# Performance work log

Measured on AMD Instinct MI355X. Metric: run time of the kernel, lower is better.

## Reference

```python
import jax, jax.numpy as jnp
import numpy as np

D_MODEL = 1024
PATCH = 16
HID = 256
VOCAB = 256

def setup_inputs() -> dict:
    key = jax.random.key(0)
    ks = jax.random.split(key, 12)
    B, N = 16, 512
    s = lambda *sh: 1.0 / np.sqrt(sh[-1])
    inp = {
        'latents': jax.random.normal(ks[0], (B, N, D_MODEL), dtype=jnp.float32),
        'target_bytes': jax.random.randint(ks[1], (B, N * PATCH), 0, VOCAB, dtype=jnp.int64),
        'W_proj': jax.random.normal(ks[2], (HID, D_MODEL), dtype=jnp.float32) * s(HID, D_MODEL),
        'b_proj': jnp.zeros((HID,), dtype=jnp.float32),
        'emb_table': jax.random.normal(ks[3], (VOCAB, HID), dtype=jnp.float32),
        'W_ih': jax.random.normal(ks[4], (3 * HID, 2 * HID), dtype=jnp.float32) * s(1, 2 * HID),
        'W_hh': jax.random.normal(ks[5], (3 * HID, HID), dtype=jnp.float32) * s(1, HID),
        'b_ih': jnp.zeros((3 * HID,), dtype=jnp.float32),
        'b_hh': jnp.zeros((3 * HID,), dtype=jnp.float32),
        'W_head': jax.random.normal(ks[6], (VOCAB, HID), dtype=jnp.float32) * s(VOCAB, HID),
        'b_head': jnp.zeros((VOCAB,), dtype=jnp.float32),
    }
    return inp

def _gru_scan(x_proj, W_hh, b_hh, h0):
    # x_proj: [T, BN, 3H] precomputed input projections (incl. b_ih)
    def step(h, xg):
        hg = h @ W_hh.T + b_hh                      # [BN, 3H]
        xr, xz, xn = jnp.split(xg, 3, axis=-1)
        hr, hz, hn = jnp.split(hg, 3, axis=-1)
        r = jax.nn.sigmoid(xr + hr)
        z = jax.nn.sigmoid(xz + hz)
        n = jnp.tanh(xn + r * hn)
        h_new = (1.0 - z) * n + z * h
        return h_new, h_new
    _, outs = jax.lax.scan(step, h0, x_proj)
    return outs                                      # [T, BN, H]

def reference(latents, target_bytes, W_proj, b_proj, emb_table, W_ih, W_hh, b_ih, b_hh, W_head, b_head):
    B, N, D = latents.shape
    BN = B * N
    latent_ctx = (latents.reshape(BN, D) @ W_proj.T + b_proj)        # [BN, H]
    targets = target_bytes.reshape(BN, PATCH)
    sos = jnp.zeros((BN, 1), dtype=targets.dtype)
    rnn_in_bytes = jnp.concatenate([sos, targets[:, :-1]], axis=1)   # [BN, P]
    emb = emb_table[rnn_in_bytes]                                    # [BN, P, H]
    lat_exp = jnp.broadcast_to(latent_ctx[:, None, :], (BN, PATCH, HID))
    rnn_input = jnp.concatenate([emb, lat_exp], axis=-1)             # [BN, P, 2H]
    x_proj = jnp.einsum('bpi,gi->bpg', rnn_input, W_ih) + b_ih       # [BN, P, 3H]
    h0 = jnp.zeros((BN, HID), dtype=latents.dtype)
    outs = _gru_scan(jnp.swapaxes(x_proj, 0, 1), W_hh, b_hh, h0)     # [P, BN, H]
    outs = jnp.swapaxes(outs, 0, 1)                                  # [BN, P, H]
    logits = jnp.einsum('bph,vh->bpv', outs, W_head) + b_head        # [BN, P, 256]
    return logits.reshape(B, N, PATCH, VOCAB)
```

## Files before the change

### kernel.cpp

```cpp
#include <hip/hip_runtime.h>
#include <math.h>

#define NSEQ 8192
#define PATCHL 16
#define HIDN 256
#define VOCABN 256

typedef __attribute__((ext_vector_type(4))) float f32x4;
typedef __attribute__((ext_vector_type(8))) short bf16x8;

__device__ __forceinline__ unsigned short f2bf(float f) {
    unsigned int x = __float_as_uint(f);
    unsigned int r = (x + 0x7fffu + ((x >> 16) & 1u)) >> 16;
    return (unsigned short)r;
}
__device__ __forceinline__ float bf2f(unsigned short b) {
    return __uint_as_float(((unsigned int)b) << 16);
}
__device__ __forceinline__ float sigf(float x)   { return 1.f / (1.f + __expf(-x)); }
__device__ __forceinline__ float tanhf_(float x) { return 2.f / (1.f + __expf(-2.f * x)) - 1.f; }

__global__ __launch_bounds__(256)
void pack_frag(const float* __restrict__ src, int ld, int col0, int nks,
               unsigned short* __restrict__ dst)
{
    const int g = blockIdx.x * 256 + threadIdx.x;
    const int lane = g & 63;
    const int ks = (g / 64) % nks;
    const int T  = g / (64 * nks);
    const float* s = src + (size_t)(T * 16 + (lane & 15)) * ld + col0 + ks * 32 + ((lane >> 4) & 3) * 8;
    unsigned int q[4];
#pragma unroll
    for (int j = 0; j < 4; j++) {
        unsigned int lo = f2bf(s[2 * j]);
        unsigned int hi = f2bf(s[2 * j + 1]);
        q[j] = lo | (hi << 16);
    }
    uint4 v; v.x = q[0]; v.y = q[1]; v.z = q[2]; v.w = q[3];
    *(uint4*)(dst + (size_t)g * 8) = v;
}

template<bool ASRC_BF16, int OUT_MODE>
__global__ __launch_bounds__(512)
void gemm_mfma(const void* __restrict__ Asrc, int lda,
               const unsigned short* __restrict__ bpack, int nks_total,
               const float* __restrict__ bias, void* __restrict__ Cdst, int ldc,
               int K)
{
    const int tid = threadIdx.x;
    const int w = tid >> 6, lane = tid & 63;
    const int l15 = lane & 15, kg = (lane >> 4) & 3;
    const int bm = blockIdx.x * 128, bn = blockIdx.y * 64;

    __shared__ unsigned short As[2][128 * 64];

    const int srow = tid >> 2;
    const int scol = (tid & 3) * 16;
    const int nkt = K / 64;

    f32x4 acc[4];
#pragma unroll
    for (int nt = 0; nt < 4; nt++) acc[nt] = 0.f;

    const int wb0 = srow * 128 + ((scol * 2) ^ ((srow & 7) << 4));
    const int wb1 = srow * 128 + ((scol * 2 + 16) ^ ((srow & 7) << 4));

#define STAGE(kt, buf) do {                                                         \
        const int gk = (kt) * 64 + scol;                                            \
        unsigned short tmp[16];                                                     \
        if (ASRC_BF16) {                                                            \
            const unsigned short* A = (const unsigned short*)Asrc;                  \
            *(uint4*)(tmp)     = *(const uint4*)(A + (size_t)(bm + srow) * lda + gk);      \
            *(uint4*)(tmp + 8) = *(const uint4*)(A + (size_t)(bm + srow) * lda + gk + 8);  \
        } else {                                                                    \
            const float* A = (const float*)Asrc;                                    \
            const float4 a0 = *(const float4*)(A + (size_t)(bm + srow) * lda + gk);       \
            const float4 a1 = *(const float4*)(A + (size_t)(bm + srow) * lda + gk + 4);   \
            const float4 a2 = *(const float4*)(A + (size_t)(bm + srow) * lda + gk + 8);   \
            const float4 a3 = *(const float4*)(A + (size_t)(bm + srow) * lda + gk + 12);  \
            tmp[0] = f2bf(a0.x);  tmp[1] = f2bf(a0.y);  tmp[2] = f2bf(a0.z);  tmp[3] = f2bf(a0.w);   \
            tmp[4] = f2bf(a1.x);  tmp[5] = f2bf(a1.y);  tmp[6] = f2bf(a1.z);  tmp[7] = f2bf(a1.w);   \
            tmp[8] = f2bf(a2.x);  tmp[9] = f2bf(a2.y);  tmp[10] = f2bf(a2.z); tmp[11] = f2bf(a2.w);  \
            tmp[12] = f2bf(a3.x); tmp[13] = f2bf(a3.y); tmp[14] = f2bf(a3.z); tmp[15] = f2bf(a3.w);  \
        }                                                                           \
        *(uint4*)((char*)As[buf] + wb0) = *(uint4*)tmp;                             \
        *(uint4*)((char*)As[buf] + wb1) = *(uint4*)(tmp + 8);                       \
    } while (0)

    STAGE(0, 0);
    __syncthreads();

    for (int kt = 0; kt < nkt; ++kt) {
        if (kt + 1 < nkt) STAGE(kt + 1, (kt + 1) & 1);
        const unsigned short* buf = As[kt & 1];
        const int row = w * 16 + l15;
#pragma unroll
        for (int ks = 0; ks < 2; ++ks) {
            const int bo = row * 128 + (((ks * 64) + kg * 16) ^ ((row & 7) << 4));
            const bf16x8 a = *(const bf16x8*)((const char*)buf + bo);
#pragma unroll
            for (int nt = 0; nt < 4; ++nt) {
                const int T = blockIdx.y * 4 + nt;
                const bf16x8 b = *(const bf16x8*)(bpack + (((size_t)T * nks_total + (kt * 2 + ks)) * 64 + lane) * 8);
                acc[nt] = __builtin_amdgcn_mfma_f32_16x16x32_bf16(a, b, acc[nt], 0, 0, 0);
            }
        }
        __syncthreads();
    }
#undef STAGE

#pragma unroll
    for (int nt = 0; nt < 4; ++nt) {
        const int n = bn + nt * 16 + l15;
        const float bv = bias ? bias[n] : 0.f;
#pragma unroll
        for (int rr = 0; rr < 4; ++rr) {
            const int m = bm + w * 16 + kg * 4 + rr;
            const float v = acc[nt][rr] + bv;
            if (OUT_MODE == 0)      ((float*)Cdst)[(size_t)m * ldc + n] = v;
            else if (OUT_MODE == 1) ((unsigned short*)Cdst)[(size_t)m * ldc + n] = f2bf(v);
            else                    ((unsigned short*)Cdst)[(size_t)m * 1024 + (n & 255) * 4 + (n >> 8)] = f2bf(v);
        }
    }
}

#define G4S 1032
__global__ __launch_bounds__(512)
void gru_scan_fused(const int* __restrict__ bytes,
                    const unsigned short* __restrict__ latg4,
                    const unsigned short* __restrict__ pmx4,
                    const unsigned short* __restrict__ wpack,
                    const unsigned short* __restrict__ hpack,
                    const float* __restrict__ b_hh,
                    const float* __restrict__ b_head,
                    float* __restrict__ out)
{
    const int tid  = threadIdx.x;
    const int w    = tid >> 6;
    const int lane = tid & 63;
    const int l15  = lane & 15;
    const int kg   = (lane >> 4) & 3;
    const int s0   = blockIdx.x * 32;

    __shared__ unsigned short H0[32 * 256];
    __shared__ unsigned short H1[32 * 256];
    __shared__ unsigned short LG[32 * G4S];
    __shared__ int BYs[512];

    BYs[tid] = bytes[(size_t)s0 * PATCHL + tid];

#pragma unroll
    for (int j = 0; j < 8; ++j) {
        const int idx = j * 512 + tid;
        const int row = idx >> 7, col = idx & 127;
        *(uint4*)(LG + row * G4S + col * 8) =
            *(const uint4*)(latg4 + (size_t)(s0 + row) * 1024 + col * 8);
    }

    float bhr[2], bhz[2], bhn[2], bhd[2];
#pragma unroll
    for (int nt = 0; nt < 2; nt++) {
        const int u = w * 32 + nt * 16 + l15;
        bhr[nt] = b_hh[u]; bhz[nt] = b_hh[256 + u]; bhn[nt] = b_hh[512 + u];
        bhd[nt] = b_head[u];
    }

    float hreg[2][2][4];
#pragma unroll
    for (int mt = 0; mt < 2; mt++)
#pragma unroll
        for (int nt = 0; nt < 2; nt++)
#pragma unroll
            for (int rr = 0; rr < 4; rr++) hreg[mt][nt][rr] = 0.f;

    unsigned short* Hcur = H0;
    unsigned short* Hnxt = H1;

    __syncthreads();

#define MFMA_TILES(pk, tbase, Hb, acc) do {                                         \
        _Pragma("unroll")                                                           \
        for (int ks = 0; ks < 8; ks += 2) {                                         \
            bf16x8 B[2][2];                                                         \
            _Pragma("unroll")                                                       \
            for (int dk = 0; dk < 2; ++dk)                                          \
                _Pragma("unroll")                                                   \
                for (int nt = 0; nt < 2; ++nt) {                                    \
                    const int T = (tbase) + w * 2 + nt;                             \
                    B[dk][nt] = *(const bf16x8*)((pk) + (((size_t)T * 8 + ks + dk) * 64 + lane) * 8); \
                }                                                                   \
            _Pragma("unroll")                                                       \
            for (int dk = 0; dk < 2; ++dk)                                          \
                _Pragma("unroll")                                                   \
                for (int mt = 0; mt < 2; ++mt) {                                    \
                    const int s = mt * 16 + l15;                                    \
                    const int off = ((ks + dk) * 64 + kg * 16) ^ ((l15 & 7) << 4);  \
                    const bf16x8 a = *(const bf16x8*)((Hb) + s * 256 + (off >> 1)); \
                    _Pragma("unroll")                                               \
                    for (int nt = 0; nt < 2; ++nt)                                  \
                        acc[mt][nt] = __builtin_amdgcn_mfma_f32_16x16x32_bf16(a, B[dk][nt], acc[mt][nt], 0, 0, 0); \
                }                                                                   \
        }                                                                           \
    } while (0)

#define HEAD_STORE(pp, Hb) do {                                                     \
        f32x4 acch[2][2];                                                           \
        _Pragma("unroll")                                                           \
        for (int mt = 0; mt < 2; mt++)                                              \
            _Pragma("unroll")                                                       \
            for (int nt = 0; nt < 2; nt++) acch[mt][nt] = 0.f;                      \
        MFMA_TILES(hpack, 0, Hb, acch);                                             \
        _Pragma("unroll")                                                           \
        for (int mt = 0; mt < 2; mt++)                                              \
            _Pragma("unroll")                                                       \
            for (int nt = 0; nt < 2; nt++) {                                        \
                const int u = w * 32 + nt * 16 + l15;                               \
                _Pragma("unroll")                                                   \
                for (int rr = 0; rr < 4; rr++) {                                    \
                    const int sl = mt * 16 + kg * 4 + rr;                           \
                    out[((size_t)(s0 + sl) * PATCHL + (pp)) * VOCABN + u] =         \
                        acch[mt][nt][rr] + bhd[nt];                                 \
                }                                                                   \
            }                                                                       \
    } while (0)

    for (int p = 0; p < PATCHL; ++p) {
        ushort4 pmreg[2][2][4];
#pragma unroll
        for (int mt = 0; mt < 2; mt++)
#pragma unroll
            for (int nt = 0; nt < 2; nt++) {
                const int u = w * 32 + nt * 16 + l15;
#pragma unroll
                for (int rr = 0; rr < 4; rr++) {
                    const int sl = mt * 16 + kg * 4 + rr;
                    const int bv = p ? BYs[sl * PATCHL + p - 1] : 0;
                    pmreg[mt][nt][rr] = *(const ushort4*)(pmx4 + (size_t)bv * 1024 + u * 4);
                }
            }

        if (p) HEAD_STORE(p - 1, Hcur);

        f32x4 acc[2][2];
#pragma unroll
        for (int mt = 0; mt < 2; mt++)
#pragma unroll
            for (int nt = 0; nt < 2; nt++) acc[mt][nt] = 0.f;
        if (p) MFMA_TILES(wpack, 0, Hcur, acc);

        float rv[2][2][4], xz[2][2][4], xn[2][2][4];
#pragma unroll
        for (int mt = 0; mt < 2; mt++)
#pragma unroll
            for (int nt = 0; nt < 2; nt++) {
                const int u = w * 32 + nt * 16 + l15;
#pragma unroll
                for (int rr = 0; rr < 4; rr++) {
                    const int sl = mt * 16 + kg * 4 + rr;
                    const ushort4 lg4 = *(const ushort4*)(LG + sl * G4S + u * 4);
                    const ushort4 pm4 = pmreg[mt][nt][rr];
                    const float xr = bf2f(lg4.x) + bf2f(pm4.x) + bhr[nt];
                    rv[mt][nt][rr] = sigf(xr + acc[mt][nt][rr]);
                    xz[mt][nt][rr] = bf2f(lg4.y) + bf2f(pm4.y) + bhz[nt];
                    xn[mt][nt][rr] = bf2f(lg4.z) + bf2f(pm4.z);
                }
            }

#pragma unroll
        for (int mt = 0; mt < 2; mt++)
#pragma unroll
            for (int nt = 0; nt < 2; nt++) acc[mt][nt] = 0.f;
        if (p) MFMA_TILES(wpack, 16, Hcur, acc);

        float zv[2][2][4];
#pragma unroll
        for (int mt = 0; mt < 2; mt++)
#pragma unroll
            for (int nt = 0; nt < 2; nt++)
#pragma unroll
                for (int rr = 0; rr < 4; rr++)
                    zv[mt][nt][rr] = sigf(xz[mt][nt][rr] + acc[mt][nt][rr]);

#pragma unroll
        for (int mt = 0; mt < 2; mt++)
#pragma unroll
            for (int nt = 0; nt < 2; nt++) acc[mt][nt] = 0.f;
        if (p) MFMA_TILES(wpack, 32, Hcur, acc);

#pragma unroll
        for (int mt = 0; mt < 2; mt++)
#pragma unroll
            for (int nt = 0; nt < 2; nt++) {
                const int u = w * 32 + nt * 16 + l15;
#pragma unroll
                for (int rr = 0; rr < 4; rr++) {
                    const int sl = mt * 16 + kg * 4 + rr;
                    const float n = tanhf_(xn[mt][nt][rr] + rv[mt][nt][rr] * (acc[mt][nt][rr] + bhn[nt]));
                    const float hn_ = (1.f - zv[mt][nt][rr]) * n + zv[mt][nt][rr] * hreg[mt][nt][rr];
                    hreg[mt][nt][rr] = hn_;
                    const int bo = (2 * u) ^ ((sl & 7) << 4);
                    Hnxt[sl * 256 + (bo >> 1)] = f2bf(hn_);
                }
            }
        __syncthreads();
        unsigned short* t_ = Hcur; Hcur = Hnxt; Hnxt = t_;
    }

    HEAD_STORE(PATCHL - 1, Hcur);
#undef HEAD_STORE
#undef MFMA_TILES
}

extern "C" void kernel_launch(void* const* d_in, const int* in_sizes, int n_in,
                              void* d_out, int out_size, void* d_ws, size_t ws_size,
                              hipStream_t stream)
{
    const float* latents = (const float*)d_in[0];
    const int*   tb      = (const int*)d_in[1];
    const float* W_proj  = (const float*)d_in[2];
    const float* b_proj  = (const float*)d_in[3];
    const float* emb     = (const float*)d_in[4];
    const float* W_ih    = (const float*)d_in[5];
    const float* W_hh    = (const float*)d_in[6];
    const float* b_ih    = (const float*)d_in[7];
    const float* b_hh    = (const float*)d_in[8];
    const float* W_head  = (const float*)d_in[9];
    const float* b_head  = (const float*)d_in[10];
    float* out = (float*)d_out;

    char* w = (char*)d_ws;
    unsigned short* latg4   = (unsigned short*)w;          w += (size_t)NSEQ * 1024 * 2;
    unsigned short* ctxb    = (unsigned short*)w;          w += (size_t)NSEQ * HIDN * 2;
    unsigned short* pmx4    = (unsigned short*)w;          w += 256 * 1024 * 2;
    unsigned short* bpack1  = (unsigned short*)w;          w += 16 * 32 * 64 * 8 * 2;
    unsigned short* bpack2  = (unsigned short*)w;          w += 48 * 8 * 64 * 8 * 2;
    unsigned short* bpack3  = (unsigned short*)w;          w += 48 * 8 * 64 * 8 * 2;
    unsigned short* wpackG  = (unsigned short*)w;          w += 48 * 8 * 64 * 8 * 2;
    unsigned short* bpackH  = (unsigned short*)w;          w += 16 * 8 * 64 * 8 * 2;

    hipLaunchKernelGGL(pack_frag, dim3(128), dim3(256), 0, stream, W_proj, 1024, 0, 32, bpack1);
    hipLaunchKernelGGL(pack_frag, dim3(96),  dim3(256), 0, stream, W_ih,   512, 256, 8, bpack2);
    hipLaunchKernelGGL(pack_frag, dim3(96),  dim3(256), 0, stream, W_ih,   512, 0,   8, bpack3);
    hipLaunchKernelGGL(pack_frag, dim3(96),  dim3(256), 0, stream, W_hh,   256, 0,   8, wpackG);
    hipLaunchKernelGGL(pack_frag, dim3(32),  dim3(256), 0, stream, W_head, 256, 0,   8, bpackH);

    hipLaunchKernelGGL((gemm_mfma<false, 2>), dim3(2, 12), dim3(512), 0, stream,
                       emb, 256, bpack3, 8, nullptr, pmx4, 1024, 256);
    hipLaunchKernelGGL((gemm_mfma<false, 1>), dim3(NSEQ / 128, 4), dim3(512), 0, stream,
                       latents, 1024, bpack1, 32, b_proj, ctxb, 256, 1024);
    hipLaunchKernelGGL((gemm_mfma<true, 2>), dim3(NSEQ / 128, 12), dim3(512), 0, stream,
                       ctxb, 256, bpack2, 8, b_ih, latg4, 1024, 256);

    hipLaunchKernelGGL(gru_scan_fused, dim3(NSEQ / 32), dim3(512), 0, stream,
                       tb, latg4, pmx4, wpackG, bpackH, b_hh, b_head, out);
}
```

Before: 375.3 us.

## Shrink GRU scan blocks to 16 sequences with 4 waves per block

The fused GRU scan kernel now processes 16 sequences per block with 256 threads instead of 32 sequences with 512 threads. Each wave covers 64 hidden units (4 N-tiles) and a single 16-row M-tile, so each loaded weight fragment now feeds one A row-tile instead of two. The aim is to double the grid (512 blocks), cut LDS per block so more blocks fit per CU, and shorten the per-step barrier. The cost is that weight fragments are re-read from memory by twice as many blocks per step, with less reuse per load.

```diff
diff --git a/kernel.cpp b/kernel.cpp
--- a/kernel.cpp
+++ b/kernel.cpp
@@ -125,7 +125,7 @@
 }
 
 #define G4S 1032
-__global__ __launch_bounds__(512)
+__global__ __launch_bounds__(256)
 void gru_scan_fused(const int* __restrict__ bytes,
                     const unsigned short* __restrict__ latg4,
                     const unsigned short* __restrict__ pmx4,
@@ -140,38 +140,36 @@
     const int lane = tid & 63;
     const int l15  = lane & 15;
     const int kg   = (lane >> 4) & 3;
-    const int s0   = blockIdx.x * 32;
-
-    __shared__ unsigned short H0[32 * 256];
-    __shared__ unsigned short H1[32 * 256];
-    __shared__ unsigned short LG[32 * G4S];
-    __shared__ int BYs[512];
+    const int s0   = blockIdx.x * 16;
+
+    __shared__ unsigned short H0[16 * 256];
+    __shared__ unsigned short H1[16 * 256];
+    __shared__ unsigned short LG[16 * G4S];
+    __shared__ int BYs[256];
 
     BYs[tid] = bytes[(size_t)s0 * PATCHL + tid];
 
 #pragma unroll
     for (int j = 0; j < 8; ++j) {
-        const int idx = j * 512 + tid;
+        const int idx = j * 256 + tid;
         const int row = idx >> 7, col = idx & 127;
         *(uint4*)(LG + row * G4S + col * 8) =
             *(const uint4*)(latg4 + (size_t)(s0 + row) * 1024 + col * 8);
     }
 
-    float bhr[2], bhz[2], bhn[2], bhd[2];
-#pragma unroll
-    for (int nt = 0; nt < 2; nt++) {
-        const int u = w * 32 + nt * 16 + l15;
+    float bhr[4], bhz[4], bhn[4], bhd[4];
+#pragma unroll
+    for (int nt = 0; nt < 4; nt++) {
+        const int u = w * 64 + nt * 16 + l15;
         bhr[nt] = b_hh[u]; bhz[nt] = b_hh[256 + u]; bhn[nt] = b_hh[512 + u];
         bhd[nt] = b_head[u];
     }
 
-    float hreg[2][2][4];
-#pragma unroll
-    for (int mt = 0; mt < 2; mt++)
-#pragma unroll
-        for (int nt = 0; nt < 2; nt++)
-#pragma unroll
-            for (int rr = 0; rr < 4; rr++) hreg[mt][nt][rr] = 0.f;
+    float hreg[4][4];
+#pragma unroll
+    for (int nt = 0; nt < 4; nt++)
+#pragma unroll
+        for (int rr = 0; rr < 4; rr++) hreg[nt][rr] = 0.f;
 
     unsigned short* Hcur = H0;
     unsigned short* Hnxt = H1;
@@ -181,127 +179,106 @@
 #define MFMA_TILES(pk, tbase, Hb, acc) do {                                         \
         _Pragma("unroll")                                                           \
         for (int ks = 0; ks < 8; ks += 2) {                                         \
-            bf16x8 B[2][2];                                                         \
+            bf16x8 B[2][4];                                                         \
             _Pragma("unroll")                                                       \
             for (int dk = 0; dk < 2; ++dk)                                          \
                 _Pragma("unroll")                                                   \
-                for (int nt = 0; nt < 2; ++nt) {                                    \
-                    const int T = (tbase) + w * 2 + nt;                             \
+                for (int nt = 0; nt < 4; ++nt) {                                    \
+                    const int T = (tbase) + w * 4 + nt;                             \
                     B[dk][nt] = *(const bf16x8*)((pk) + (((size_t)T * 8 + ks + dk) * 64 + lane) * 8); \
                 }                                                                   \
             _Pragma("unroll")                                                       \
-            for (int dk = 0; dk < 2; ++dk)                                          \
+            for (int dk = 0; dk < 2; ++dk) {                                        \
+                const int off = ((ks + dk) * 64 + kg * 16) ^ ((l15 & 7) << 4);      \
+                const bf16x8 a = *(const bf16x8*)((Hb) + l15 * 256 + (off >> 1));   \
                 _Pragma("unroll")                                                   \
-                for (int mt = 0; mt < 2; ++mt) {                                    \
-                    const int s = mt * 16 + l15;                                    \
-                    const int off = ((ks + dk) * 64 + kg * 16) ^ ((l15 & 7) << 4);  \
-                    const bf16x8 a = *(const bf16x8*)((Hb) + s * 256 + (off >> 1)); \
-                    _Pragma("unroll")                                               \
-                    for (int nt = 0; nt < 2; ++nt)                                  \
-                        acc[mt][nt] = __builtin_amdgcn_mfma_f32_16x16x32_bf16(a, B[dk][nt], acc[mt][nt], 0, 0, 0); \
-                }                                                                   \
+                for (int nt = 0; nt < 4; ++nt)                                      \
+                    acc[nt] = __builtin_amdgcn_mfma_f32_16x16x32_bf16(a, B[dk][nt], acc[nt], 0, 0, 0); \
+            }                                                                       \
         }                                                                           \
     } while (0)
 
 #define HEAD_STORE(pp, Hb) do {                                                     \
-        f32x4 acch[2][2];                                                           \
+        f32x4 acch[4];                                                              \
         _Pragma("unroll")                                                           \
-        for (int mt = 0; mt < 2; mt++)                                              \
-            _Pragma("unroll")                                                       \
-            for (int nt = 0; nt < 2; nt++) acch[mt][nt] = 0.f;                      \
+        for (int nt = 0; nt < 4; nt++) acch[nt] = 0.f;                              \
         MFMA_TILES(hpack, 0, Hb, acch);                                             \
         _Pragma("unroll")                                                           \
-        for (int mt = 0; mt < 2; mt++)                                              \
+        for (int nt = 0; nt < 4; nt++) {                                            \
+            const int u = w * 64 + nt * 16 + l15;                                   \
             _Pragma("unroll")                                                       \
-            for (int nt = 0; nt < 2; nt++) {                                        \
-                const int u = w * 32 + nt * 16 + l15;                               \
-                _Pragma("unroll")                                                   \
-                for (int rr = 0; rr < 4; rr++) {                                    \
-                    const int sl = mt * 16 + kg * 4 + rr;                           \
-                    out[((size_t)(s0 + sl) * PATCHL + (pp)) * VOCABN + u] =         \
-                        acch[mt][nt][rr] + bhd[nt];                                 \
-                }                                                                   \
+            for (int rr = 0; rr < 4; rr++) {                                        \
+                const int sl = kg * 4 + rr;                                         \
+                out[((size_t)(s0 + sl) * PATCHL + (pp)) * VOCABN + u] =             \
+                    acch[nt][rr] + bhd[nt];                                         \
             }                                                                       \
+        }                                                                           \
     } while (0)
 
     for (int p = 0; p < PATCHL; ++p) {
-        ushort4 pmreg[2][2][4];
-#pragma unroll
-        for (int mt = 0; mt < 2; mt++)
-#pragma unroll
-            for (int nt = 0; nt < 2; nt++) {
-                const int u = w * 32 + nt * 16 + l15;
-#pragma unroll
-                for (int rr = 0; rr < 4; rr++) {
-                    const int sl = mt * 16 + kg * 4 + rr;
-                    const int bv = p ? BYs[sl * PATCHL + p - 1] : 0;
-                    pmreg[mt][nt][rr] = *(const ushort4*)(pmx4 + (size_t)bv * 1024 + u * 4);
-                }
+        ushort4 pmreg[4][4];
+#pragma unroll
+        for (int nt = 0; nt < 4; nt++) {
+            const int u = w * 64 + nt * 16 + l15;
+#pragma unroll
+            for (int rr = 0; rr < 4; rr++) {
+                const int sl = kg * 4 + rr;
+                const int bv = p ? BYs[sl * PATCHL + p - 1] : 0;
+                pmreg[nt][rr] = *(const ushort4*)(pmx4 + (size_t)bv * 1024 + u * 4);
             }
+        }
 
         if (p) HEAD_STORE(p - 1, Hcur);
 
-        f32x4 acc[2][2];
-#pragma unroll
-        for (int mt = 0; mt < 2; mt++)
-#pragma unroll
-            for (int nt = 0; nt < 2; nt++) acc[mt][nt] = 0.f;
+        f32x4 acc[4];
+#pragma unroll
+        for (int nt = 0; nt < 4; nt++) acc[nt] = 0.f;
         if (p) MFMA_TILES(wpack, 0, Hcur, acc);
 
-        float rv[2][2][4], xz[2][2][4], xn[2][2][4];
-#pragma unroll
-        for (int mt = 0; mt < 2; mt++)
-#pragma unroll
-            for (int nt = 0; nt < 2; nt++) {
-                const int u = w * 32 + nt * 16 + l15;
-#pragma unroll
-                for (int rr = 0; rr < 4; rr++) {
-                    const int sl = mt * 16 + kg * 4 + rr;
-                    const ushort4 lg4 = *(const ushort4*)(LG + sl * G4S + u * 4);
-                    const ushort4 pm4 = pmreg[mt][nt][rr];
-                    const float xr = bf2f(lg4.x) + bf2f(pm4.x) + bhr[nt];
-                    rv[mt][nt][rr] = sigf(xr + acc[mt][nt][rr]);
-                    xz[mt][nt][rr] = bf2f(lg4.y) + bf2f(pm4.y) + bhz[nt];
-                    xn[mt][nt][rr] = bf2f(lg4.z) + bf2f(pm4.z);
-                }
+        float rv[4][4], xz[4][4], xn[4][4];
+#pragma unroll
+        for (int nt = 0; nt < 4; nt++) {
+            const int u = w * 64 + nt * 16 + l15;
+#pragma unroll
+            for (int rr = 0; rr < 4; rr++) {
+                const int sl = kg * 4 + rr;
+                const ushort4 lg4 = *(const ushort4*)(LG + sl * G4S + u * 4);
+                const ushort4 pm4 = pmreg[nt][rr];
+                const float xr = bf2f(lg4.x) + bf2f(pm4.x) + bhr[nt];
+                rv[nt][rr] = sigf(xr + acc[nt][rr]);
+                xz[nt][rr] = bf2f(lg4.y) + bf2f(pm4.y) + bhz[nt];
+                xn[nt][rr] = bf2f(lg4.z) + bf2f(pm4.z);
             }
-
-#pragma unroll
-        for (int mt = 0; mt < 2; mt++)
-#pragma unroll
-            for (int nt = 0; nt < 2; nt++) acc[mt][nt] = 0.f;
+        }
+
+#pragma unroll
+        for (int nt = 0; nt < 4; nt++) acc[nt] = 0.f;
         if (p) MFMA_TILES(wpack, 16, Hcur, acc);
 
-        float zv[2][2][4];
-#pragma unroll
-        for (int mt = 0; mt < 2; mt++)
-#pragma unroll
-            for (int nt = 0; nt < 2; nt++)
-#pragma unroll
-                for (int rr = 0; rr < 4; rr++)
-                    zv[mt][nt][rr] = sigf(xz[mt][nt][rr] + acc[mt][nt][rr]);
-
-#pragma unroll
-        for (int mt = 0; mt < 2; mt++)
-#pragma unroll
-            for (int nt = 0; nt < 2; nt++) acc[mt][nt] = 0.f;
+        float zv[4][4];
+#pragma unroll
+        for (int nt = 0; nt < 4; nt++)
+#pragma unroll
+            for (int rr = 0; rr < 4; rr++)
+                zv[nt][rr] = sigf(xz[nt][rr] + acc[nt][rr]);
+
+#pragma unroll
+        for (int nt = 0; nt < 4; nt++) acc[nt] = 0.f;
         if (p) MFMA_TILES(wpack, 32, Hcur, acc);
 
 #pragma unroll
-        for (int mt = 0; mt < 2; mt++)
-#pragma unroll
-            for (int nt = 0; nt < 2; nt++) {
-                const int u = w * 32 + nt * 16 + l15;
-#pragma unroll
-                for (int rr = 0; rr < 4; rr++) {
-                    const int sl = mt * 16 + kg * 4 + rr;
-                    const float n = tanhf_(xn[mt][nt][rr] + rv[mt][nt][rr] * (acc[mt][nt][rr] + bhn[nt]));
-                    const float hn_ = (1.f - zv[mt][nt][rr]) * n + zv[mt][nt][rr] * hreg[mt][nt][rr];
-                    hreg[mt][nt][rr] = hn_;
-                    const int bo = (2 * u) ^ ((sl & 7) << 4);
-                    Hnxt[sl * 256 + (bo >> 1)] = f2bf(hn_);
-                }
+        for (int nt = 0; nt < 4; nt++) {
+            const int u = w * 64 + nt * 16 + l15;
+#pragma unroll
+            for (int rr = 0; rr < 4; rr++) {
+                const int sl = kg * 4 + rr;
+                const float n = tanhf_(xn[nt][rr] + rv[nt][rr] * (acc[nt][rr] + bhn[nt]));
+                const float hn_ = (1.f - zv[nt][rr]) * n + zv[nt][rr] * hreg[nt][rr];
+                hreg[nt][rr] = hn_;
+                const int bo = (2 * u) ^ ((sl & 7) << 4);
+                Hnxt[sl * 256 + (bo >> 1)] = f2bf(hn_);
             }
+        }
         __syncthreads();
         unsigned short* t_ = Hcur; Hcur = Hnxt; Hnxt = t_;
     }
@@ -351,6 +328,6 @@
     hipLaunchKernelGGL((gemm_mfma<true, 2>), dim3(NSEQ / 128, 12), dim3(512), 0, stream,
                        ctxb, 256, bpack2, 8, b_ih, latg4, 1024, 256);
 
-    hipLaunchKernelGGL(gru_scan_fused, dim3(NSEQ / 32), dim3(512), 0, stream,
+    hipLaunchKernelGGL(gru_scan_fused, dim3(NSEQ / 16), dim3(256), 0, stream,
                        tb, latg4, pmx4, wpackG, bpackH, b_hh, b_head, out);
 }
```

New measurement: 389.3 us. +3.7%, slower.
